# Optimization experiments

Hardware: AMD Instinct MI355X
Metric: run time of the kernel (lower is better)

Reference implementation:

```python
import jax, jax.numpy as jnp
import numpy as np

W_MODE, W_COMFORT, W_PROGRESS, W_COLLISION, W_DRIVABLE = 1.0, 0.1, 0.5, 1.0, 0.3
COLLISION_RADIUS = 2.0
LANE_MAX_DIST = 3.0
BIG = 1000000.0


def setup_inputs() -> dict:
    key = jax.random.key(0)
    k1, k2, k3, k4 = jax.random.split(key, 4)
    B, M, T = 16, 60, 80
    N_AGENTS, N_LANES, N_PTS = 128, 64, 20
    return {
        "mode_logits": jax.random.normal(k1, (B, M), dtype=jnp.float32),
        "all_trajs": jax.random.normal(k2, (B, M, T, 3), dtype=jnp.float32),
        "agents_now": jax.random.normal(k3, (B, N_AGENTS, 4), dtype=jnp.float32),
        "agents_mask": jnp.ones((B, N_AGENTS), dtype=jnp.float32),
        "map_lanes": jax.random.normal(k4, (B, N_LANES, N_PTS, 3), dtype=jnp.float32),
        "map_lanes_mask": jnp.ones((B, N_LANES), dtype=jnp.float32),
    }


def reference(mode_logits, all_trajs, agents_now, agents_mask, map_lanes, map_lanes_mask):
    B, M, T, _ = all_trajs.shape
    mode_scores = jax.nn.softmax(mode_logits, axis=-1)  # (B, M)

    ego_xy = all_trajs[..., :2]  # (B, M, T, 2)

    # Comfort: mean jerk norm (3rd finite difference of position)
    vel = ego_xy[:, :, 1:] - ego_xy[:, :, :-1]
    acc = vel[:, :, 1:] - vel[:, :, :-1]
    jerk = acc[:, :, 1:] - acc[:, :, :-1]
    comfort = -jnp.linalg.norm(jerk, axis=-1).mean(axis=-1)  # (B, M)

    # Progress: final x-coordinate
    progress = all_trajs[:, :, -1, 0]  # (B, M)

    # Collision: fraction of timesteps within radius of any valid agent
    agent_xy = agents_now[:, :, :2]  # (B, N, 2)
    # (B, M, T, N): pairwise distance ego trajectory points vs agents
    d_ag = jnp.linalg.norm(ego_xy[:, :, :, None, :] - agent_xy[:, None, None, :, :], axis=-1)
    d_ag = d_ag + (1.0 - agents_mask[:, None, None, :]) * BIG
    min_dist = d_ag.min(axis=-1)  # (B, M, T)
    collision = -(min_dist < COLLISION_RADIUS).astype(jnp.float32).mean(axis=-1)  # (B, M)

    # Drivable: fraction of timesteps farther than lane_max_dist from any valid lane point
    B_, L, P, _ = map_lanes.shape
    lane_flat = map_lanes[..., :2].reshape(B, L * P, 2)  # (B, L*P, 2)
    lane_valid_flat = jnp.repeat(map_lanes_mask, P, axis=1)  # (B, L*P)
    d_ln = jnp.linalg.norm(ego_xy[:, :, :, None, :] - lane_flat[:, None, None, :, :], axis=-1)
    d_ln = d_ln + (1.0 - lane_valid_flat[:, None, None, :]) * BIG
    min_lane_dist = d_ln.min(axis=-1)  # (B, M, T)
    drivable = -(min_lane_dist > LANE_MAX_DIST).astype(jnp.float32).mean(axis=-1)  # (B, M)

    score = (W_MODE * mode_scores + W_COMFORT * comfort + W_PROGRESS * progress
             + W_COLLISION * collision + W_DRIVABLE * drivable)  # (B, M)
    selected_idx = jnp.argmax(score, axis=1)  # (B,)
    selected_traj = all_trajs[jnp.arange(B), selected_idx]  # (B, T, 3)
    return selected_traj, selected_idx
```

## Files before the change

kernel.cpp:

```cpp
#include <hip/hip_runtime.h>
#include <math.h>

#define BM 60
#define TT 80
#define NAG 128
#define NLANES 64
#define NPTS 20
#define NLP (NLANES * NPTS)
#define PPL (NLP / 64)
#define APL (NAG / 64)

__global__ __launch_bounds__(256) void score_kernel(
    const float* __restrict__ trajs,
    const float* __restrict__ agents,
    const float* __restrict__ amask,
    const float* __restrict__ lanes,
    const float* __restrict__ lmask,
    float* __restrict__ scores)
{
    __shared__ float s_ex[TT], s_ey[TT];
    __shared__ float s_j[2];
    __shared__ float s_cc[4], s_cd[4];

    const int bm   = blockIdx.x;
    const int b    = bm / BM;
    const int tid  = threadIdx.x;
    const int w    = tid >> 6;
    const int lane = tid & 63;

    const float* tr = trajs + (size_t)bm * TT * 3;
    for (int i = tid; i < TT; i += 256) {
        s_ex[i] = tr[i * 3 + 0];
        s_ey[i] = tr[i * 3 + 1];
    }

    float ax[APL], ay[APL], aq[APL];
#pragma unroll
    for (int k = 0; k < APL; ++k) {
        const int i = lane + 64 * k;
        const float off = (1.0f - amask[b * NAG + i]) * 1e8f;
        const float x = agents[((size_t)b * NAG + i) * 4 + 0] + off;
        const float y = agents[((size_t)b * NAG + i) * 4 + 1];
        ax[k] = x; ay[k] = y; aq[k] = fmaf(x, x, y * y);
    }
    float px[PPL], py[PPL], pq[PPL];
#pragma unroll
    for (int k = 0; k < PPL; ++k) {
        const int i = lane + 64 * k;
        const float off = (1.0f - lmask[b * NLANES + i / NPTS]) * 1e8f;
        const float x = lanes[((size_t)b * NLP + i) * 3 + 0] + off;
        const float y = lanes[((size_t)b * NLP + i) * 3 + 1];
        px[k] = x; py[k] = y; pq[k] = fmaf(x, x, y * y);
    }

    __syncthreads();

    float jsum = 0.0f;
    if (tid < TT - 3) {
        const float jx = s_ex[tid + 3] - 3.0f * s_ex[tid + 2] + 3.0f * s_ex[tid + 1] - s_ex[tid];
        const float jy = s_ey[tid + 3] - 3.0f * s_ey[tid + 2] + 3.0f * s_ey[tid + 1] - s_ey[tid];
        jsum = sqrtf(jx * jx + jy * jy);
    }
    for (int off = 32; off > 0; off >>= 1) jsum += __shfl_xor(jsum, off, 64);
    if (w < 2 && lane == 0) s_j[w] = jsum;

    int ccoll = 0, cdriv = 0;
    const int t0 = w * (TT / 4);
    for (int r = 0; r < 4; ++r) {
        const int tb = t0 + r * 5;
        float mx5[5], my5[5], thrA[5], thrB[5], m2[5], m3[5];
#pragma unroll
        for (int j = 0; j < 5; ++j) {
            const float ex = s_ex[tb + j];
            const float ey = s_ey[tb + j];
            const float c  = fmaf(ex, ex, ey * ey);
            mx5[j]  = -2.0f * ex;
            my5[j]  = -2.0f * ey;
            thrA[j] = 4.0f - c;
            thrB[j] = 9.0f - c;
            m2[j] = 1e30f;
            m3[j] = 1e30f;
        }
#pragma unroll
        for (int k = 0; k < APL; ++k) {
#pragma unroll
            for (int j = 0; j < 5; ++j) {
                float v = fmaf(my5[j], ay[k], aq[k]);
                v = fmaf(mx5[j], ax[k], v);
                m2[j] = fminf(m2[j], v);
            }
        }
#pragma unroll
        for (int k = 0; k < PPL; ++k) {
#pragma unroll
            for (int j = 0; j < 5; ++j) {
                float v = fmaf(my5[j], py[k], pq[k]);
                v = fmaf(mx5[j], px[k], v);
                m3[j] = fminf(m3[j], v);
            }
        }
#pragma unroll
        for (int j = 0; j < 5; ++j) {
            ccoll += (__ballot(m2[j] < thrA[j]) != 0ull) ? 1 : 0;
            cdriv += (__ballot(m3[j] <= thrB[j]) == 0ull) ? 1 : 0;
        }
    }
    if (lane == 0) { s_cc[w] = (float)ccoll; s_cd[w] = (float)cdriv; }
    __syncthreads();

    if (tid == 0) {
        const float coll = s_cc[0] + s_cc[1] + s_cc[2] + s_cc[3];
        const float driv = s_cd[0] + s_cd[1] + s_cd[2] + s_cd[3];
        const float comfort  = -((s_j[0] + s_j[1]) / (float)(TT - 3));
        const float progress = tr[(TT - 1) * 3 + 0];
        scores[bm] = 0.1f * comfort + 0.5f * progress
                   - 1.0f * (coll / (float)TT)
                   - 0.3f * (driv / (float)TT);
    }
}

__global__ __launch_bounds__(64) void select_kernel(
    const float* __restrict__ logits,
    const float* __restrict__ trajs,
    const float* __restrict__ scores,
    float* __restrict__ out,
    int B)
{
    const int b    = blockIdx.x;
    const int lane = threadIdx.x;

    float lg = (lane < BM) ? logits[b * BM + lane] : -1e30f;
    float mx = lg;
    for (int off = 32; off > 0; off >>= 1) mx = fmaxf(mx, __shfl_xor(mx, off, 64));
    float e = (lane < BM) ? expf(lg - mx) : 0.0f;
    float sum = e;
    for (int off = 32; off > 0; off >>= 1) sum += __shfl_xor(sum, off, 64);

    float sc = (lane < BM) ? (e / sum + scores[b * BM + lane]) : -1e30f;
    int idx = lane;
    for (int off = 32; off > 0; off >>= 1) {
        float os = __shfl_xor(sc, off, 64);
        int   oi = __shfl_xor(idx, off, 64);
        if (os > sc || (os == sc && oi < idx)) { sc = os; idx = oi; }
    }
    const float* src = trajs + ((size_t)b * BM + idx) * TT * 3;
    for (int k = lane; k < TT * 3; k += 64) out[b * TT * 3 + k] = src[k];
    if (lane == 0) out[B * TT * 3 + b] = (float)idx;
}

extern "C" void kernel_launch(void* const* d_in, const int* in_sizes, int n_in,
                              void* d_out, int out_size, void* d_ws, size_t ws_size,
                              hipStream_t stream) {
    const float* logits = (const float*)d_in[0];
    const float* trajs  = (const float*)d_in[1];
    const float* agents = (const float*)d_in[2];
    const float* amask  = (const float*)d_in[3];
    const float* lanes  = (const float*)d_in[4];
    const float* lmask  = (const float*)d_in[5];

    const int B = in_sizes[0] / BM;
    float* scores = (float*)d_ws;
    float* out    = (float*)d_out;

    score_kernel<<<B * BM, 256, 0, stream>>>(trajs, agents, amask, lanes, lmask, scores);
    select_kernel<<<B, 64, 0, stream>>>(logits, trajs, scores, out, B);
}
```

Baseline: 78.27 us.

## Replace full min-distance sweeps with ballot-based early-exit threshold checks

Instead of computing the full minimum distance to all agents and lane points, each wave now tests the threshold per timestep with a ballot and stops scanning lane chunks once any point is within range. Lane points are staged in shared memory rather than registers, and agents are loaded with vector loads. This is meant to cut the bulk of the distance arithmetic on typical data. In exchange it adds data-dependent branching, a serial per-timestep ballot loop and more LDS traffic.

```diff
diff --git a/kernel.cpp b/kernel.cpp
--- a/kernel.cpp
+++ b/kernel.cpp
@@ -7,8 +7,7 @@
 #define NLANES 64
 #define NPTS 20
 #define NLP (NLANES * NPTS)
-#define PPL (NLP / 64)
-#define APL (NAG / 64)
+#define BIGOFF 1e8f
 
 __global__ __launch_bounds__(256) void score_kernel(
     const float* __restrict__ trajs,
@@ -18,6 +17,7 @@
     const float* __restrict__ lmask,
     float* __restrict__ scores)
 {
+    __shared__ float s_px[NLP], s_py[NLP];
     __shared__ float s_ex[TT], s_ey[TT];
     __shared__ float s_j[2];
     __shared__ float s_cc[4], s_cd[4];
@@ -30,29 +30,25 @@
 
     const float* tr = trajs + (size_t)bm * TT * 3;
     for (int i = tid; i < TT; i += 256) {
-        s_ex[i] = tr[i * 3 + 0];
-        s_ey[i] = tr[i * 3 + 1];
+        s_ex[i] = tr[3 * i];
+        s_ey[i] = tr[3 * i + 1];
     }
-
-    float ax[APL], ay[APL], aq[APL];
-#pragma unroll
-    for (int k = 0; k < APL; ++k) {
-        const int i = lane + 64 * k;
-        const float off = (1.0f - amask[b * NAG + i]) * 1e8f;
-        const float x = agents[((size_t)b * NAG + i) * 4 + 0] + off;
-        const float y = agents[((size_t)b * NAG + i) * 4 + 1];
-        ax[k] = x; ay[k] = y; aq[k] = fmaf(x, x, y * y);
+    const float* lbase = lanes + (size_t)b * NLP * 3;
+    for (int p = tid; p < NLP; p += 256) {
+        const float off = (1.0f - lmask[b * NLANES + p / NPTS]) * BIGOFF;
+        s_px[p] = lbase[3 * p] + off;
+        s_py[p] = lbase[3 * p + 1];
     }
-    float px[PPL], py[PPL], pq[PPL];
-#pragma unroll
-    for (int k = 0; k < PPL; ++k) {
-        const int i = lane + 64 * k;
-        const float off = (1.0f - lmask[b * NLANES + i / NPTS]) * 1e8f;
-        const float x = lanes[((size_t)b * NLP + i) * 3 + 0] + off;
-        const float y = lanes[((size_t)b * NLP + i) * 3 + 1];
-        px[k] = x; py[k] = y; pq[k] = fmaf(x, x, y * y);
+    float ax0, ay0, ax1, ay1;
+    {
+        const float4* ga4 = (const float4*)(agents + (size_t)b * NAG * 4);
+        const float4 a0 = ga4[lane];
+        const float4 a1 = ga4[64 + lane];
+        ax0 = a0.x + (1.0f - amask[b * NAG + lane]) * BIGOFF;
+        ay0 = a0.y;
+        ax1 = a1.x + (1.0f - amask[b * NAG + 64 + lane]) * BIGOFF;
+        ay1 = a1.y;
     }
-
     __syncthreads();
 
     float jsum = 0.0f;
@@ -66,43 +62,28 @@
 
     int ccoll = 0, cdriv = 0;
     const int t0 = w * (TT / 4);
-    for (int r = 0; r < 4; ++r) {
-        const int tb = t0 + r * 5;
-        float mx5[5], my5[5], thrA[5], thrB[5], m2[5], m3[5];
-#pragma unroll
-        for (int j = 0; j < 5; ++j) {
-            const float ex = s_ex[tb + j];
-            const float ey = s_ey[tb + j];
-            const float c  = fmaf(ex, ex, ey * ey);
-            mx5[j]  = -2.0f * ex;
-            my5[j]  = -2.0f * ey;
-            thrA[j] = 4.0f - c;
-            thrB[j] = 9.0f - c;
-            m2[j] = 1e30f;
-            m3[j] = 1e30f;
+    for (int t = t0; t < t0 + TT / 4; ++t) {
+        const float ex = s_ex[t], ey = s_ey[t];
+
+        {
+            float dx = ex - ax0, dy = ey - ay0;
+            unsigned long long m = __ballot(fmaf(dx, dx, dy * dy) < 4.0f);
+            if (m == 0ull) {
+                dx = ex - ax1; dy = ey - ay1;
+                m = __ballot(fmaf(dx, dx, dy * dy) < 4.0f);
+            }
+            ccoll += (m != 0ull) ? 1 : 0;
         }
-#pragma unroll
-        for (int k = 0; k < APL; ++k) {
-#pragma unroll
-            for (int j = 0; j < 5; ++j) {
-                float v = fmaf(my5[j], ay[k], aq[k]);
-                v = fmaf(mx5[j], ax[k], v);
-                m2[j] = fminf(m2[j], v);
+        {
+            unsigned long long m = 0ull;
+            for (int k = 0; k < NLP / 64; ++k) {
+                const int p = k * 64 + lane;
+                const float dx = ex - s_px[p];
+                const float dy = ey - s_py[p];
+                m = __ballot(fmaf(dx, dx, dy * dy) <= 9.0f);
+                if (m != 0ull) break;
             }
-        }
-#pragma unroll
-        for (int k = 0; k < PPL; ++k) {
-#pragma unroll
-            for (int j = 0; j < 5; ++j) {
-                float v = fmaf(my5[j], py[k], pq[k]);
-                v = fmaf(mx5[j], px[k], v);
-                m3[j] = fminf(m3[j], v);
-            }
-        }
-#pragma unroll
-        for (int j = 0; j < 5; ++j) {
-            ccoll += (__ballot(m2[j] < thrA[j]) != 0ull) ? 1 : 0;
-            cdriv += (__ballot(m3[j] <= thrB[j]) == 0ull) ? 1 : 0;
+            cdriv += (m == 0ull) ? 1 : 0;
         }
     }
     if (lane == 0) { s_cc[w] = (float)ccoll; s_cd[w] = (float)cdriv; }
@@ -112,7 +93,7 @@
         const float coll = s_cc[0] + s_cc[1] + s_cc[2] + s_cc[3];
         const float driv = s_cd[0] + s_cd[1] + s_cd[2] + s_cd[3];
         const float comfort  = -((s_j[0] + s_j[1]) / (float)(TT - 3));
-        const float progress = tr[(TT - 1) * 3 + 0];
+        const float progress = s_ex[TT - 1];
         scores[bm] = 0.1f * comfort + 0.5f * progress
                    - 1.0f * (coll / (float)TT)
                    - 0.3f * (driv / (float)TT);
```

Measured after the change: 71.04 us. 1.1x faster.
